# Optimization experiments

Measured on AMD Instinct MI355X. Metric: run time of the kernel, lower is better.

Reference implementation:

```python
import jax, jax.numpy as jnp
import numpy as np

TOP_K_PERCENT = 0.7


def setup_inputs() -> dict:
    key = jax.random.key(0)
    k1, k2, k3, k4 = jax.random.split(key, 4)
    B, C, H, W = 4, 19, 512, 1024
    logits = jax.random.normal(k1, (B, C, H, W), dtype=jnp.float32)
    labels = jax.random.randint(k2, (B, H, W), 0, C, dtype=jnp.int64)
    smooth_labels = jax.random.uniform(k3, (B, C, H, W), dtype=jnp.float32)
    weight2 = jax.random.uniform(k4, (C,), dtype=jnp.float32)
    return {"logits": logits, "labels": labels, "smooth_labels": smooth_labels, "weight2": weight2}


def reference(logits, labels, smooth_labels, weight2):
    # Fused equivalent of the per-class loop:
    #   cum[b,h,w] = sum_c smooth[b,c,h,w] * weight2[c] * (-log_softmax(logits)[b,c,h,w])
    # (ignore_label=-1 never matches any class index, so no masking occurs.)
    logp = jax.nn.log_softmax(logits, axis=1)  # [B,C,H,W]
    w = weight2[None, :, None, None]
    pixel_losses_2 = -(smooth_labels * w * logp).sum(axis=1)  # [B,H,W]
    flat = pixel_losses_2.reshape(-1)
    k = int(TOP_K_PERCENT * flat.shape[0])  # static shape -> python int
    top_vals, _ = jax.lax.top_k(flat, k)
    return top_vals.mean()
```

## Files before the change

### kernel.cpp

```cpp
#include <hip/hip_runtime.h>

#define NPIX 2097152
#define NT4  524288
#define NCH  19
#define CPL4 131072
#define KSEL 1468006u
#define LBLK 2048
#define HB   512
#define NCP  8
#define H1B  4096
#define H2B  1024

#define OFF_COMB1 (NPIX*4)
#define OFF_COMB2 (OFF_COMB1 + NCP*H1B*4)
#define OFF_COMB3 (OFF_COMB2 + NCP*H2B*4)
#define OFF_PART  (OFF_COMB3 + NCP*H2B*4)
#define OFF_CTRL  (OFF_PART + HB*8)
#define ZBYTES    (NCP*(H1B + H2B + H2B)*4)

__global__ __launch_bounds__(256, 8) void k_loss(
    const float* __restrict__ logits, const float* __restrict__ smooth,
    const float* __restrict__ wgt, float* __restrict__ loss,
    unsigned* __restrict__ comb1)
{
    __shared__ unsigned h[H1B];
    for (int j = threadIdx.x; j < H1B; j += 256) h[j] = 0u;

    int tid = blockIdx.x * 256 + threadIdx.x;
    int img = tid >> 17;
    int rem = tid & (CPL4 - 1);
    const float4* L = (const float4*)logits + (size_t)img * (NCH * CPL4) + rem;
    const float4* S = (const float4*)smooth + (size_t)img * (NCH * CPL4) + rem;

    float4 xb[3], sb[3];
    #pragma unroll
    for (int i = 0; i < 3; ++i) {
        xb[i] = L[(size_t)i * CPL4];
        sb[i] = S[(size_t)i * CPL4];
    }
    __syncthreads();

    float s0 = 0.f, s1 = 0.f, s2 = 0.f, s3 = 0.f;
    float sw0 = 0.f, sw1 = 0.f, sw2 = 0.f, sw3 = 0.f;
    float swl0 = 0.f, swl1 = 0.f, swl2 = 0.f, swl3 = 0.f;

    #pragma unroll
    for (int c = 0; c < NCH; ++c) {
        float4 xv = xb[c % 3];
        float4 sv = sb[c % 3];
        if (c + 3 < NCH) {
            xb[c % 3] = L[(size_t)(c + 3) * CPL4];
            sb[c % 3] = S[(size_t)(c + 3) * CPL4];
        }
        float wc = wgt[c];
        s0 += __expf(xv.x); s1 += __expf(xv.y);
        s2 += __expf(xv.z); s3 += __expf(xv.w);
        float t0 = sv.x * wc, t1 = sv.y * wc, t2 = sv.z * wc, t3 = sv.w * wc;
        sw0 += t0; sw1 += t1; sw2 += t2; sw3 += t3;
        swl0 = fmaf(t0, xv.x, swl0); swl1 = fmaf(t1, xv.y, swl1);
        swl2 = fmaf(t2, xv.z, swl2); swl3 = fmaf(t3, xv.w, swl3);
    }

    float l0 = fmaxf(__logf(s0) * sw0 - swl0, 0.f);
    float l1 = fmaxf(__logf(s1) * sw1 - swl1, 0.f);
    float l2 = fmaxf(__logf(s2) * sw2 - swl2, 0.f);
    float l3 = fmaxf(__logf(s3) * sw3 - swl3, 0.f);
    ((float4*)loss)[tid] = make_float4(l0, l1, l2, l3);

    atomicAdd(&h[__float_as_uint(l0) >> 20], 1u);
    atomicAdd(&h[__float_as_uint(l1) >> 20], 1u);
    atomicAdd(&h[__float_as_uint(l2) >> 20], 1u);
    atomicAdd(&h[__float_as_uint(l3) >> 20], 1u);
    __syncthreads();

    unsigned* dst = comb1 + (size_t)(blockIdx.x & (NCP - 1)) * H1B;
    for (int j = threadIdx.x; j < H1B; j += 256) {
        unsigned c = h[j];
        if (c) atomicAdd(&dst[j], c);
    }
}

__device__ __forceinline__ void suffix_select(
    unsigned* h, unsigned* cs, unsigned* shv, int cpt, unsigned need)
{
    int t = threadIdx.x;
    unsigned sum = 0;
    for (int j = 0; j < cpt; ++j) sum += h[t * cpt + j];
    cs[t] = sum;
    __syncthreads();
    for (int off = 1; off < 256; off <<= 1) {
        unsigned v = (t + off < 256) ? cs[t + off] : 0u;
        __syncthreads();
        cs[t] += v;
        __syncthreads();
    }
    unsigned St = cs[t], Sn = (t < 255) ? cs[t + 1] : 0u;
    if (St >= need && Sn < need) { shv[0] = (unsigned)t; shv[1] = Sn; }
    __syncthreads();
    if (t == 0) {
        unsigned cum = shv[1];
        for (int bb = (int)shv[0] * cpt + cpt - 1;; --bb) {
            unsigned c = h[bb];
            if (cum + c >= need) { shv[2] = (unsigned)bb; shv[3] = need - cum; break; }
            cum += c;
        }
    }
    __syncthreads();
}

__global__ __launch_bounds__(256) void k_h2(
    const uint4* __restrict__ lb, const unsigned* __restrict__ comb1,
    unsigned* __restrict__ comb2, unsigned* __restrict__ ctrl)
{
    __shared__ unsigned bins[H1B];
    __shared__ unsigned cs[256];
    __shared__ unsigned shv[4];
    int t = threadIdx.x, b = blockIdx.x;

    for (int j = t; j < H1B; j += 256) {
        unsigned s = 0;
        #pragma unroll
        for (int cp = 0; cp < NCP; ++cp) s += comb1[(size_t)cp * H1B + j];
        bins[j] = s;
    }
    __syncthreads();
    suffix_select(bins, cs, shv, H1B / 256, KSEL);
    unsigned p1 = shv[2], n1 = shv[3];
    if (b == 0 && t == 0) { ctrl[0] = p1; ctrl[1] = n1; }

    for (int j = t; j < H2B; j += 256) bins[j] = 0u;
    __syncthreads();
    int base = b * 256 + t;
    #pragma unroll
    for (int k = 0; k < NT4 / (HB * 256); ++k) {
        uint4 v = lb[(size_t)k * (HB * 256) + base];
        if ((v.x >> 20) == p1) atomicAdd(&bins[(v.x >> 10) & 1023u], 1u);
        if ((v.y >> 20) == p1) atomicAdd(&bins[(v.y >> 10) & 1023u], 1u);
        if ((v.z >> 20) == p1) atomicAdd(&bins[(v.z >> 10) & 1023u], 1u);
        if ((v.w >> 20) == p1) atomicAdd(&bins[(v.w >> 10) & 1023u], 1u);
    }
    __syncthreads();
    unsigned* dst = comb2 + (size_t)(b & (NCP - 1)) * H2B;
    for (int j = t; j < H2B; j += 256)
        if (bins[j]) atomicAdd(&dst[j], bins[j]);
}

__global__ __launch_bounds__(256) void k_h3(
    const uint4* __restrict__ lb, const unsigned* __restrict__ comb2,
    unsigned* __restrict__ comb3, double* __restrict__ partials,
    unsigned* __restrict__ ctrl)
{
    __shared__ unsigned bins[H2B];
    __shared__ unsigned cs[256];
    __shared__ unsigned shv[4];
    __shared__ double wsum[4];
    int t = threadIdx.x, b = blockIdx.x;
    unsigned p1 = ctrl[0], n1 = ctrl[1];

    for (int j = t; j < H2B; j += 256) {
        unsigned s = 0;
        #pragma unroll
        for (int cp = 0; cp < NCP; ++cp) s += comb2[(size_t)cp * H2B + j];
        bins[j] = s;
    }
    __syncthreads();
    suffix_select(bins, cs, shv, H2B / 256, n1);
    unsigned p2 = (p1 << 10) | shv[2], n2 = shv[3];
    if (b == 0 && t == 0) { ctrl[2] = p2; ctrl[3] = n2; }

    for (int j = t; j < H2B; j += 256) bins[j] = 0u;
    __syncthreads();
    double acc = 0.0;
    int base = b * 256 + t;
    #pragma unroll
    for (int k = 0; k < NT4 / (HB * 256); ++k) {
        uint4 v = lb[(size_t)k * (HB * 256) + base];
        unsigned px = v.x >> 10, py = v.y >> 10, pz = v.z >> 10, pw = v.w >> 10;
        if (px == p2) atomicAdd(&bins[v.x & 1023u], 1u);
        else if (px > p2) acc += (double)__uint_as_float(v.x);
        if (py == p2) atomicAdd(&bins[v.y & 1023u], 1u);
        else if (py > p2) acc += (double)__uint_as_float(v.y);
        if (pz == p2) atomicAdd(&bins[v.z & 1023u], 1u);
        else if (pz > p2) acc += (double)__uint_as_float(v.z);
        if (pw == p2) atomicAdd(&bins[v.w & 1023u], 1u);
        else if (pw > p2) acc += (double)__uint_as_float(v.w);
    }
    __syncthreads();
    unsigned* dst = comb3 + (size_t)(b & (NCP - 1)) * H2B;
    for (int j = t; j < H2B; j += 256)
        if (bins[j]) atomicAdd(&dst[j], bins[j]);

    #pragma unroll
    for (int off = 32; off > 0; off >>= 1) acc += __shfl_down(acc, off, 64);
    if ((t & 63) == 0) wsum[t >> 6] = acc;
    __syncthreads();
    if (t == 0) partials[b] = wsum[0] + wsum[1] + wsum[2] + wsum[3];
}

__global__ __launch_bounds__(256) void k_fin(
    const unsigned* __restrict__ comb3, const double* __restrict__ partials,
    const unsigned* __restrict__ ctrl, float* __restrict__ out)
{
    __shared__ unsigned bins[H2B];
    __shared__ unsigned cs[256];
    __shared__ unsigned shv[4];
    __shared__ double wsum[4];
    int t = threadIdx.x;
    unsigned p2 = ctrl[2], n2 = ctrl[3];

    for (int j = t; j < H2B; j += 256) {
        unsigned s = 0;
        #pragma unroll
        for (int cp = 0; cp < NCP; ++cp) s += comb3[(size_t)cp * H2B + j];
        bins[j] = s;
    }
    __syncthreads();
    suffix_select(bins, cs, shv, H2B / 256, n2);
    unsigned b3 = shv[2], r2 = shv[3];

    double acc = partials[t] + partials[t + 256];
    #pragma unroll
    for (int kk = 0; kk < 4; ++kk) {
        int bb = t * 4 + kk;
        if (bb > (int)b3 && bins[bb])
            acc += (double)bins[bb] * (double)__uint_as_float((p2 << 10) | (unsigned)bb);
    }
    #pragma unroll
    for (int off = 32; off > 0; off >>= 1) acc += __shfl_down(acc, off, 64);
    if ((t & 63) == 0) wsum[t >> 6] = acc;
    __syncthreads();
    if (t == 0) {
        double tot = wsum[0] + wsum[1] + wsum[2] + wsum[3];
        tot += (double)r2 * (double)__uint_as_float((p2 << 10) | b3);
        out[0] = (float)(tot / (double)KSEL);
    }
}

extern "C" void kernel_launch(void* const* d_in, const int* in_sizes, int n_in,
                              void* d_out, int out_size, void* d_ws, size_t ws_size,
                              hipStream_t stream)
{
    const float* logits = (const float*)d_in[0];
    const float* smooth = (const float*)d_in[2];
    const float* wgt    = (const float*)d_in[3];

    char* ws = (char*)d_ws;
    float*    loss     = (float*)ws;
    unsigned* comb1    = (unsigned*)(ws + OFF_COMB1);
    unsigned* comb2    = (unsigned*)(ws + OFF_COMB2);
    unsigned* comb3    = (unsigned*)(ws + OFF_COMB3);
    double*   partials = (double*)(ws + OFF_PART);
    unsigned* ctrl     = (unsigned*)(ws + OFF_CTRL);
    const uint4* lb    = (const uint4*)loss;

    hipMemsetAsync(ws + OFF_COMB1, 0, ZBYTES, stream);
    k_loss<<<LBLK, 256, 0, stream>>>(logits, smooth, wgt, loss, comb1);
    k_h2  <<<HB,   256, 0, stream>>>(lb, comb1, comb2, ctrl);
    k_h3  <<<HB,   256, 0, stream>>>(lb, comb2, comb3, partials, ctrl);
    k_fin <<<1,    256, 0, stream>>>(comb3, partials, ctrl, (float*)d_out);
}
```

Baseline: 352.1 us.

## Fold final select into k_h3 via last-block ticket; use 1024-thread loss blocks

Removes the separate single-block finalize kernel by having the last k_h3 block (detected via an atomic ticket counter zeroed by the existing memset) perform the final histogram select and mean. It also enlarges k_loss blocks from 256 to 1024 threads, so each shared 4096-bin histogram is flushed to global by a quarter as many blocks. This saves one kernel launch and the global histogram atomic traffic, but relies on threadfence/atomic-load ordering and lower per-block occupancy flexibility in k_loss.

```diff
diff --git a/kernel.cpp b/kernel.cpp
--- a/kernel.cpp
+++ b/kernel.cpp
@@ -5,7 +5,8 @@
 #define NCH  19
 #define CPL4 131072
 #define KSEL 1468006u
-#define LBLK 2048
+#define LBS  1024
+#define LBLK (NT4/LBS)
 #define HB   512
 #define NCP  8
 #define H1B  4096
@@ -14,19 +15,20 @@
 #define OFF_COMB1 (NPIX*4)
 #define OFF_COMB2 (OFF_COMB1 + NCP*H1B*4)
 #define OFF_COMB3 (OFF_COMB2 + NCP*H2B*4)
-#define OFF_PART  (OFF_COMB3 + NCP*H2B*4)
+#define OFF_TICK  (OFF_COMB3 + NCP*H2B*4)
+#define OFF_PART  (OFF_TICK + 16)
 #define OFF_CTRL  (OFF_PART + HB*8)
-#define ZBYTES    (NCP*(H1B + H2B + H2B)*4)
-
-__global__ __launch_bounds__(256, 8) void k_loss(
+#define ZBYTES    (OFF_TICK + 16 - OFF_COMB1)
+
+__global__ __launch_bounds__(LBS) void k_loss(
     const float* __restrict__ logits, const float* __restrict__ smooth,
     const float* __restrict__ wgt, float* __restrict__ loss,
     unsigned* __restrict__ comb1)
 {
     __shared__ unsigned h[H1B];
-    for (int j = threadIdx.x; j < H1B; j += 256) h[j] = 0u;
-
-    int tid = blockIdx.x * 256 + threadIdx.x;
+    for (int j = threadIdx.x; j < H1B; j += LBS) h[j] = 0u;
+
+    int tid = blockIdx.x * LBS + threadIdx.x;
     int img = tid >> 17;
     int rem = tid & (CPL4 - 1);
     const float4* L = (const float4*)logits + (size_t)img * (NCH * CPL4) + rem;
@@ -74,7 +76,7 @@
     __syncthreads();
 
     unsigned* dst = comb1 + (size_t)(blockIdx.x & (NCP - 1)) * H1B;
-    for (int j = threadIdx.x; j < H1B; j += 256) {
+    for (int j = threadIdx.x; j < H1B; j += LBS) {
         unsigned c = h[j];
         if (c) atomicAdd(&dst[j], c);
     }
@@ -108,6 +110,8 @@
     __syncthreads();
 }
 
+#define ALD(p)  __hip_atomic_load((p), __ATOMIC_RELAXED, __HIP_MEMORY_SCOPE_AGENT)
+
 __global__ __launch_bounds__(256) void k_h2(
     const uint4* __restrict__ lb, const unsigned* __restrict__ comb1,
     unsigned* __restrict__ comb2, unsigned* __restrict__ ctrl)
@@ -148,12 +152,14 @@
 __global__ __launch_bounds__(256) void k_h3(
     const uint4* __restrict__ lb, const unsigned* __restrict__ comb2,
     unsigned* __restrict__ comb3, double* __restrict__ partials,
-    unsigned* __restrict__ ctrl)
+    const unsigned* __restrict__ ctrl, unsigned* __restrict__ ticket,
+    float* __restrict__ out)
 {
     __shared__ unsigned bins[H2B];
     __shared__ unsigned cs[256];
     __shared__ unsigned shv[4];
     __shared__ double wsum[4];
+    __shared__ unsigned sh_last;
     int t = threadIdx.x, b = blockIdx.x;
     unsigned p1 = ctrl[0], n1 = ctrl[1];
 
@@ -166,7 +172,6 @@
     __syncthreads();
     suffix_select(bins, cs, shv, H2B / 256, n1);
     unsigned p2 = (p1 << 10) | shv[2], n2 = shv[3];
-    if (b == 0 && t == 0) { ctrl[2] = p2; ctrl[3] = n2; }
 
     for (int j = t; j < H2B; j += 256) bins[j] = 0u;
     __syncthreads();
@@ -194,40 +199,36 @@
     for (int off = 32; off > 0; off >>= 1) acc += __shfl_down(acc, off, 64);
     if ((t & 63) == 0) wsum[t >> 6] = acc;
     __syncthreads();
-    if (t == 0) partials[b] = wsum[0] + wsum[1] + wsum[2] + wsum[3];
-}
-
-__global__ __launch_bounds__(256) void k_fin(
-    const unsigned* __restrict__ comb3, const double* __restrict__ partials,
-    const unsigned* __restrict__ ctrl, float* __restrict__ out)
-{
-    __shared__ unsigned bins[H2B];
-    __shared__ unsigned cs[256];
-    __shared__ unsigned shv[4];
-    __shared__ double wsum[4];
-    int t = threadIdx.x;
-    unsigned p2 = ctrl[2], n2 = ctrl[3];
-
+    if (t == 0) {
+        partials[b] = wsum[0] + wsum[1] + wsum[2] + wsum[3];
+        __threadfence();
+        sh_last = (atomicAdd(ticket, 1u) == HB - 1) ? 1u : 0u;
+    }
+    __syncthreads();
+    if (!sh_last) return;
+
+    __threadfence();
     for (int j = t; j < H2B; j += 256) {
         unsigned s = 0;
         #pragma unroll
-        for (int cp = 0; cp < NCP; ++cp) s += comb3[(size_t)cp * H2B + j];
+        for (int cp = 0; cp < NCP; ++cp) s += ALD(&comb3[(size_t)cp * H2B + j]);
         bins[j] = s;
     }
     __syncthreads();
     suffix_select(bins, cs, shv, H2B / 256, n2);
     unsigned b3 = shv[2], r2 = shv[3];
 
-    double acc = partials[t] + partials[t + 256];
+    double a2 = __hip_atomic_load(&partials[t], __ATOMIC_RELAXED, __HIP_MEMORY_SCOPE_AGENT)
+              + __hip_atomic_load(&partials[t + 256], __ATOMIC_RELAXED, __HIP_MEMORY_SCOPE_AGENT);
     #pragma unroll
     for (int kk = 0; kk < 4; ++kk) {
         int bb = t * 4 + kk;
         if (bb > (int)b3 && bins[bb])
-            acc += (double)bins[bb] * (double)__uint_as_float((p2 << 10) | (unsigned)bb);
-    }
-    #pragma unroll
-    for (int off = 32; off > 0; off >>= 1) acc += __shfl_down(acc, off, 64);
-    if ((t & 63) == 0) wsum[t >> 6] = acc;
+            a2 += (double)bins[bb] * (double)__uint_as_float((p2 << 10) | (unsigned)bb);
+    }
+    #pragma unroll
+    for (int off = 32; off > 0; off >>= 1) a2 += __shfl_down(a2, off, 64);
+    if ((t & 63) == 0) wsum[t >> 6] = a2;
     __syncthreads();
     if (t == 0) {
         double tot = wsum[0] + wsum[1] + wsum[2] + wsum[3];
@@ -249,13 +250,14 @@
     unsigned* comb1    = (unsigned*)(ws + OFF_COMB1);
     unsigned* comb2    = (unsigned*)(ws + OFF_COMB2);
     unsigned* comb3    = (unsigned*)(ws + OFF_COMB3);
+    unsigned* ticket   = (unsigned*)(ws + OFF_TICK);
     double*   partials = (double*)(ws + OFF_PART);
     unsigned* ctrl     = (unsigned*)(ws + OFF_CTRL);
     const uint4* lb    = (const uint4*)loss;
 
     hipMemsetAsync(ws + OFF_COMB1, 0, ZBYTES, stream);
-    k_loss<<<LBLK, 256, 0, stream>>>(logits, smooth, wgt, loss, comb1);
+    k_loss<<<LBLK, LBS, 0, stream>>>(logits, smooth, wgt, loss, comb1);
     k_h2  <<<HB,   256, 0, stream>>>(lb, comb1, comb2, ctrl);
-    k_h3  <<<HB,   256, 0, stream>>>(lb, comb2, comb3, partials, ctrl);
-    k_fin <<<1,    256, 0, stream>>>(comb3, partials, ctrl, (float*)d_out);
-}
+    k_h3  <<<HB,   256, 0, stream>>>(lb, comb2, comb3, partials, ctrl,
+                                     ticket, (float*)d_out);
+}
```

Result: slower. 361.0 us (+2.5%).
